# Performance work log

Hardware: AMD Instinct MI355X
Metric: run time of the kernel (lower is better)

Reference implementation:

```python
import jax, jax.numpy as jnp
import numpy as np
from jax import lax

L, H, DH, D, FF = 8, 16, 64, 1024, 4096  # layers, heads, head dim, model dim, mlp hidden
B, S = 4, 512
EPS = 1e-5


def setup_inputs() -> dict:
    key = jax.random.key(0)
    ks = jax.random.split(key, 8)
    std = 0.02
    return {
        "x": jax.random.normal(ks[0], (B, S, D), jnp.float32),
        "ln1_w": jnp.ones((L, D), jnp.float32),
        "ln1_b": jnp.zeros((L, D), jnp.float32),
        "qw": jax.random.normal(ks[1], (L, H, DH, DH), jnp.float32) * std,
        "qb": jnp.zeros((L, H, DH), jnp.float32),
        "kw": jax.random.normal(ks[2], (L, H, DH, DH), jnp.float32) * std,
        "kb": jnp.zeros((L, H, DH), jnp.float32),
        "vw": jax.random.normal(ks[3], (L, H, DH, DH), jnp.float32) * std,
        "vb": jnp.zeros((L, H, DH), jnp.float32),
        "ln2_w": jnp.ones((L, D), jnp.float32),
        "ln2_b": jnp.zeros((L, D), jnp.float32),
        "w1": jax.random.normal(ks[4], (L, D, FF), jnp.float32) * std,
        "b1": jnp.zeros((L, FF), jnp.float32),
        "w2": jax.random.normal(ks[5], (L, FF, D), jnp.float32) * std,
        "b2": jnp.zeros((L, D), jnp.float32),
    }


def _layernorm(x, w, b):
    m = jnp.mean(x, axis=-1, keepdims=True)
    v = jnp.mean(jnp.square(x - m), axis=-1, keepdims=True)
    return (x - m) * lax.rsqrt(v + EPS) * w + b


def reference(x, ln1_w, ln1_b, qw, qb, kw, kb, vw, vb, ln2_w, ln2_b, w1, b1, w2, b2):
    b, s, d = x.shape
    scale = 1.0 / jnp.sqrt(jnp.asarray(DH, x.dtype))

    def layer(h, p):
        (l1w, l1b, Qw, Qb, Kw, Kb, Vw, Vb, l2w, l2b, W1, B1, W2, B2) = p
        y = _layernorm(h, l1w, l1b)
        yh = y.reshape(b, s, H, DH)
        # nn.Linear per head: y @ W.T + b, W is [out=e, in=d]
        q = jnp.einsum('bshd,hed->bshe', yh, Qw) + Qb
        k = jnp.einsum('bshd,hed->bshe', yh, Kw) + Kb
        v = jnp.einsum('bshd,hed->bshe', yh, Vw) + Vb
        attn = jax.nn.softmax(jnp.einsum('bshe,bthe->bhst', q, k) * scale, axis=-1)
        o = jnp.einsum('bhst,bthe->bshe', attn, v).reshape(b, s, d)
        h = h + o
        z = _layernorm(h, l2w, l2b)
        z = jax.nn.gelu(z @ W1 + B1, approximate=False) @ W2 + B2
        return h + z, None

    params = (ln1_w, ln1_b, qw, qb, kw, kb, vw, vb, ln2_w, ln2_b, w1, b1, w2, b2)
    out, _ = lax.scan(layer, x, params)
    return out
```

## Files before the change

### kernel.cpp

```cpp
#include <hip/hip_runtime.h>
#include <hip/hip_bf16.h>

typedef __hip_bfloat16 bf16;
typedef __bf16 bf16x8 __attribute__((ext_vector_type(8)));
typedef float f32x4 __attribute__((ext_vector_type(4)));
typedef unsigned short u16;
typedef unsigned int u32;

#define SEQ 512
#define DMODEL 1024
#define FFDIM 4096
#define NHEAD 16
#define HDIM 64
#define NB 4
#define NLAYER 8

#define SBAR() asm volatile("s_barrier" ::: "memory")

__device__ __forceinline__ u16 f2bu(float f) {
    union { bf16 h; u16 u; } c; c.h = __float2bfloat16(f); return c.u;
}
__device__ __forceinline__ float bu2f(u16 u) {
    union { u32 i; float f; } c; c.i = ((u32)u) << 16; return c.f;
}

__device__ __forceinline__ void gload16(const bf16* g, bf16* l) {
    __builtin_amdgcn_global_load_lds(
        (const __attribute__((address_space(1))) unsigned int*)g,
        (__attribute__((address_space(3))) unsigned int*)l,
        16, 0, 0);
}

__device__ __forceinline__ void gemm_pipe(
    const bf16* __restrict__ A, int lda,
    const bf16* __restrict__ Bt,
    int nkt,
    f32x4 (&acc)[8][2],
    char* lA, char* lB)
{
    const int tid = threadIdx.x;
    const int lane = tid & 63;
    const int wave = tid >> 6;
    const int wr = wave >> 2, wc = wave & 3;
    const int l15 = lane & 15, l4 = lane >> 4;

    auto stage = [&](int c, int t) {
        const bf16* Ak = A + t * 64;
        bf16* dA = (bf16*)(lA + c * 32768);
        bf16* dB = (bf16*)(lB + c * 16384);
#pragma unroll
        for (int it = 0; it < 4; ++it) {
            const int e = (it * 512 + tid) * 8;
            const int r = e >> 6;
            const int cb = (e & 63) * 2;
            const int sc = (cb ^ (((r >> 2) & 1) << 5)) >> 1;
            gload16(Ak + (long)r * lda + sc, dA + e);
        }
        const bf16* Bk = Bt + (long)t * 8192;
#pragma unroll
        for (int it = 0; it < 2; ++it) {
            const int e = (it * 512 + tid) * 8;
            gload16(Bk + e, dB + e);
        }
    };

    stage(0, 0);
    stage(1, 1);
    asm volatile("s_waitcnt vmcnt(6)" ::: "memory");
    SBAR();

    for (int t = 0; t < nkt; ++t) {
        const int cur = t % 3;
        if (t + 2 < nkt) stage((t + 2) % 3, t + 2);

        const char* bA = lA + cur * 32768;
        const char* bB = lB + cur * 16384;

        bf16x8 bf_[2][2];
#pragma unroll
        for (int fn = 0; fn < 2; ++fn)
#pragma unroll
            for (int ks = 0; ks < 2; ++ks) {
                const int row = wc * 32 + fn * 16 + l15;
                int byte = row * 128 + (ks * 32 + l4 * 8) * 2;
                byte ^= ((row >> 2) & 1) << 5;
                bf_[fn][ks] = *(const bf16x8*)(bB + byte);
            }
#pragma unroll
        for (int q = 0; q < 4; ++q) {
            bf16x8 af[2][2];
#pragma unroll
            for (int i = 0; i < 2; ++i)
#pragma unroll
                for (int ks = 0; ks < 2; ++ks) {
                    const int row = wr * 128 + (q * 2 + i) * 16 + l15;
                    int byte = row * 128 + (ks * 32 + l4 * 8) * 2;
                    byte ^= ((row >> 2) & 1) << 5;
                    af[i][ks] = *(const bf16x8*)(bA + byte);
                }
            __builtin_amdgcn_s_setprio(1);
#pragma unroll
            for (int i = 0; i < 2; ++i)
#pragma unroll
                for (int fn = 0; fn < 2; ++fn)
#pragma unroll
                    for (int ks = 0; ks < 2; ++ks)
                        acc[q * 2 + i][fn] = __builtin_amdgcn_mfma_f32_16x16x32_bf16(
                            af[i][ks], bf_[fn][ks], acc[q * 2 + i][fn], 0, 0, 0);
            __builtin_amdgcn_s_setprio(0);
        }
        if (t + 2 < nkt) {
            asm volatile("s_waitcnt vmcnt(6)" ::: "memory");
        } else if (t + 1 < nkt) {
            asm volatile("s_waitcnt vmcnt(0)" ::: "memory");
        }
        SBAR();
    }
}

__global__ __launch_bounds__(256) void k_ln(const float* __restrict__ h,
                                            const float* __restrict__ w,
                                            const float* __restrict__ bp,
                                            bf16* __restrict__ out,
                                            float* __restrict__ hcopy)
{
    const int row = blockIdx.x;
    const int tid = threadIdx.x;
    const float4 x = ((const float4*)(h + (long)row * DMODEL))[tid];
    if (hcopy) ((float4*)(hcopy + (long)row * DMODEL))[tid] = x;
    float s  = x.x + x.y + x.z + x.w;
    float s2 = x.x * x.x + x.y * x.y + x.z * x.z + x.w * x.w;
#pragma unroll
    for (int off = 32; off; off >>= 1) { s += __shfl_xor(s, off); s2 += __shfl_xor(s2, off); }
    __shared__ float rs[4], rs2[4];
    const int wave = tid >> 6;
    if ((tid & 63) == 0) { rs[wave] = s; rs2[wave] = s2; }
    __syncthreads();
    const float S1 = rs[0] + rs[1] + rs[2] + rs[3];
    const float S2 = rs2[0] + rs2[1] + rs2[2] + rs2[3];
    const float mean = S1 * (1.0f / DMODEL);
    const float var  = S2 * (1.0f / DMODEL) - mean * mean;
    const float rstd = rsqrtf(var + 1e-5f);
    const float4 wv = ((const float4*)w)[tid];
    const float4 bv = ((const float4*)bp)[tid];
    uint2 o;
    o.x = (u32)f2bu((x.x - mean) * rstd * wv.x + bv.x) |
          ((u32)f2bu((x.y - mean) * rstd * wv.y + bv.y) << 16);
    o.y = (u32)f2bu((x.z - mean) * rstd * wv.z + bv.z) |
          ((u32)f2bu((x.w - mean) * rstd * wv.w + bv.w) << 16);
    ((uint2*)(out + (long)row * DMODEL))[tid] = o;
}

__global__ __launch_bounds__(256) void k_tilew(const float* __restrict__ w1,
                                               const float* __restrict__ w2,
                                               bf16* __restrict__ w1t,
                                               bf16* __restrict__ w2t)
{
    __shared__ u16 t[64][138];
    int bid = blockIdx.x;
    const int l = bid >> 10;
    bid &= 1023;
    const long lofs = (long)l * DMODEL * FFDIM;
    const float* src; bf16* dst; int ldsrc;
    if (bid < 512) {
        const int by = bid >> 4, kt = bid & 15;
        src = w1 + lofs + (long)(kt * 64) * FFDIM + by * 128;
        ldsrc = FFDIM;
        dst = w1t + lofs + ((long)by * 16 + kt) * 8192;
    } else {
        bid -= 512;
        const int by = bid >> 6, kt = bid & 63;
        src = w2 + lofs + (long)(kt * 64) * DMODEL + by * 128;
        ldsrc = DMODEL;
        dst = w2t + lofs + ((long)by * 64 + kt) * 8192;
    }
    const int tid = threadIdx.x;
    const int n4 = (tid & 31) * 4;
    const int kr = tid >> 5;
#pragma unroll
    for (int j = 0; j < 8; ++j) {
        const int k = j * 8 + kr;
        const float4 v = *(const float4*)(src + (long)k * ldsrc + n4);
        t[k][n4]     = f2bu(v.x);
        t[k][n4 + 1] = f2bu(v.y);
        t[k][n4 + 2] = f2bu(v.z);
        t[k][n4 + 3] = f2bu(v.w);
    }
    __syncthreads();
#pragma unroll
    for (int it = 0; it < 4; ++it) {
        const int e0 = it * 2048 + tid * 8;
        const int r = e0 >> 6;
        const int c = e0 & 63;
        const int ksw = c ^ (((r >> 2) & 1) << 4);
        u16 v[8];
#pragma unroll
        for (int m = 0; m < 8; ++m) v[m] = t[ksw + m][r];
        uint4 o;
        o.x = (u32)v[0] | ((u32)v[1] << 16);
        o.y = (u32)v[2] | ((u32)v[3] << 16);
        o.z = (u32)v[4] | ((u32)v[5] << 16);
        o.w = (u32)v[6] | ((u32)v[7] << 16);
        *(uint4*)(dst + e0) = o;
    }
}

__global__ __launch_bounds__(256) void k_attn(const bf16* __restrict__ y,
                                              const float* __restrict__ qwl,
                                              const float* __restrict__ kwl,
                                              const float* __restrict__ vwl,
                                              const float* __restrict__ qb,
                                              const float* __restrict__ kb,
                                              const float* __restrict__ vb,
                                              float* __restrict__ h)
{
    __shared__ __align__(16) char lmem[65536];
    bf16* lY  = (bf16*)lmem;
    char* lQ  = lmem + 16384;
    char* lK  = lmem + 32768;
    char* lV  = lmem + 40960;
    char* lWk = lmem + 49152;
    char* lWv = lmem + 57344;

    const int tid = threadIdx.x;
    const int lane = tid & 63, wave = tid >> 6;
    const int l15 = lane & 15, l4 = lane >> 4;
    const int z = blockIdx.y, b = z >> 4, hd = z & 15;
    const int q0 = blockIdx.x * 128;

    {
        const float* s0 = qwl + (long)hd * HDIM * HDIM;
        const float* s1 = kwl + (long)hd * HDIM * HDIM;
        const float* s2 = vwl + (long)hd * HDIM * HDIM;
#pragma unroll
        for (int it = 0; it < 4; ++it) {
            const int f = (it * 256 + tid) * 4;
            const int row = f >> 6;
            const int byte = (f << 1) ^ ((row & 7) << 4);
            float4 v = *(const float4*)(s0 + f);
            uint2 o;
            o.x = (u32)f2bu(v.x) | ((u32)f2bu(v.y) << 16);
            o.y = (u32)f2bu(v.z) | ((u32)f2bu(v.w) << 16);
            *(uint2*)(lK + byte) = o;
            v = *(const float4*)(s1 + f);
            o.x = (u32)f2bu(v.x) | ((u32)f2bu(v.y) << 16);
            o.y = (u32)f2bu(v.z) | ((u32)f2bu(v.w) << 16);
            *(uint2*)(lWk + byte) = o;
            v = *(const float4*)(s2 + f);
            o.x = (u32)f2bu(v.x) | ((u32)f2bu(v.y) << 16);
            o.y = (u32)f2bu(v.z) | ((u32)f2bu(v.w) << 16);
            *(uint2*)(lWv + byte) = o;
        }
    }
    const bf16* Yq = y + ((long)b * SEQ + q0) * DMODEL + hd * HDIM;
#pragma unroll
    for (int it = 0; it < 4; ++it) {
        const int e = (it * 256 + tid) * 8;
        const int r = e >> 6;
        const int cb = (e & 63) * 2;
        const int sc = (cb ^ (((r >> 2) & 1) << 5)) >> 1;
        gload16(Yq + (long)r * DMODEL + sc, lY + e);
    }
    __syncthreads();

    {
        f32x4 qacc[2][4] = {};
#pragma unroll
        for (int ks = 0; ks < 2; ++ks) {
            bf16x8 af[2];
#pragma unroll
            for (int fm = 0; fm < 2; ++fm) {
                const int row = wave * 32 + fm * 16 + l15;
                int byte = row * 128 + (ks * 32 + l4 * 8) * 2;
                byte ^= ((row >> 2) & 1) << 5;
                af[fm] = *(const bf16x8*)((char*)lY + byte);
            }
#pragma unroll
            for (int fn = 0; fn < 4; ++fn) {
                const int wrow = fn * 16 + l15;
                int wbyte = (wrow << 7) + ((ks * 32 + l4 * 8) << 1);
                wbyte ^= (wrow & 7) << 4;
                const bf16x8 wf = *(const bf16x8*)(lK + wbyte);
#pragma unroll
                for (int fm = 0; fm < 2; ++fm)
                    qacc[fm][fn] = __builtin_amdgcn_mfma_f32_16x16x32_bf16(
                        af[fm], wf, qacc[fm][fn], 0, 0, 0);
            }
        }
#pragma unroll
        for (int fm = 0; fm < 2; ++fm)
#pragma unroll
            for (int fn = 0; fn < 4; ++fn) {
                const int e = fn * 16 + l15;
                const float bias = qb[hd * HDIM + e];
#pragma unroll
                for (int r = 0; r < 4; ++r) {
                    const int row = wave * 32 + fm * 16 + l4 * 4 + r;
                    const int byte = ((row << 7) + (e << 1)) ^ ((row & 7) << 4);
                    *(u16*)(lQ + byte) = f2bu((qacc[fm][fn][r] + bias) * 0.125f);
                }
            }
    }
    __syncthreads();

    bf16x8 qa[2][2];
#pragma unroll
    for (int fm = 0; fm < 2; ++fm)
#pragma unroll
        for (int ks = 0; ks < 2; ++ks) {
            const int row = wave * 32 + fm * 16 + l15;
            int byte = (row << 7) + ((ks * 32 + l4 * 8) << 1);
            byte ^= (row & 7) << 4;
            qa[fm][ks] = *(const bf16x8*)(lQ + byte);
        }

    char* lP = lQ + wave * 4096;

    f32x4 O[2][4] = {};
    float mrun[2][4], lrun[2][4];
#pragma unroll
    for (int fm = 0; fm < 2; ++fm)
#pragma unroll
        for (int r = 0; r < 4; ++r) { mrun[fm][r] = -1e30f; lrun[fm][r] = 0.0f; }

    for (int kv = 0; kv < SEQ / 64; ++kv) {
        __syncthreads();
        const bf16* Ykv = y + ((long)b * SEQ + kv * 64) * DMODEL + hd * HDIM;
#pragma unroll
        for (int it = 0; it < 2; ++it) {
            const int e = (it * 256 + tid) * 8;
            const int r = e >> 6;
            const int cb = (e & 63) * 2;
            const int sc = (cb ^ (((r >> 2) & 1) << 5)) >> 1;
            gload16(Ykv + (long)r * DMODEL + sc, lY + e);
        }
        __syncthreads();

        {
            f32x4 kacc[4] = {}, vacc[4] = {};
#pragma unroll
            for (int ks = 0; ks < 2; ++ks) {
                const int yrow = wave * 16 + l15;
                int ybyte = yrow * 128 + (ks * 32 + l4 * 8) * 2;
                ybyte ^= ((yrow >> 2) & 1) << 5;
                const bf16x8 ay = *(const bf16x8*)((char*)lY + ybyte);
#pragma unroll
                for (int fn = 0; fn < 4; ++fn) {
                    const int wrow = fn * 16 + l15;
                    int wbyte = (wrow << 7) + ((ks * 32 + l4 * 8) << 1);
                    wbyte ^= (wrow & 7) << 4;
                    kacc[fn] = __builtin_amdgcn_mfma_f32_16x16x32_bf16(
                        ay, *(const bf16x8*)(lWk + wbyte), kacc[fn], 0, 0, 0);
                    vacc[fn] = __builtin_amdgcn_mfma_f32_16x16x32_bf16(
                        ay, *(const bf16x8*)(lWv + wbyte), vacc[fn], 0, 0, 0);
                }
            }
#pragma unroll
            for (int fn = 0; fn < 4; ++fn) {
                const int e = fn * 16 + l15;
                const float kbv = kb[hd * HDIM + e];
                const float vbv = vb[hd * HDIM + e];
#pragma unroll
                for (int r = 0; r < 4; ++r) {
                    const int key = wave * 16 + l4 * 4 + r;
                    const int kbyte = ((key << 7) + (e << 1)) ^ ((key & 7) << 4);
                    *(u16*)(lK + kbyte) = f2bu(kacc[fn][r] + kbv);
                    const int vbyte = ((e << 7) + (key << 1)) ^ ((e & 7) << 4);
                    *(u16*)(lV + vbyte) = f2bu(vacc[fn][r] + vbv);
                }
            }
        }
        __syncthreads();

        f32x4 sa[2][4];
#pragma unroll
        for (int fm = 0; fm < 2; ++fm)
#pragma unroll
            for (int fn = 0; fn < 4; ++fn) sa[fm][fn] = (f32x4){0.f, 0.f, 0.f, 0.f};
#pragma unroll
        for (int ks = 0; ks < 2; ++ks)
#pragma unroll
            for (int fn = 0; fn < 4; ++fn) {
                const int row = fn * 16 + l15;
                int byte = (row << 7) + ((ks * 32 + l4 * 8) << 1);
                byte ^= (row & 7) << 4;
                const bf16x8 kf = *(const bf16x8*)(lK + byte);
#pragma unroll
                for (int fm = 0; fm < 2; ++fm)
                    sa[fm][fn] = __builtin_amdgcn_mfma_f32_16x16x32_bf16(
                        qa[fm][ks], kf, sa[fm][fn], 0, 0, 0);
            }

#pragma unroll
        for (int fm = 0; fm < 2; ++fm)
#pragma unroll
            for (int r = 0; r < 4; ++r) {
                float mx = fmaxf(fmaxf(sa[fm][0][r], sa[fm][1][r]),
                                 fmaxf(sa[fm][2][r], sa[fm][3][r]));
#pragma unroll
                for (int m_ = 1; m_ < 16; m_ <<= 1) mx = fmaxf(mx, __shfl_xor(mx, m_));
                const float nm = fmaxf(mrun[fm][r], mx);
                const float al = __expf(mrun[fm][r] - nm);
                mrun[fm][r] = nm;
                float p0 = __expf(sa[fm][0][r] - nm), p1 = __expf(sa[fm][1][r] - nm);
                float p2 = __expf(sa[fm][2][r] - nm), p3 = __expf(sa[fm][3][r] - nm);
                float ps = p0 + p1 + p2 + p3;
#pragma unroll
                for (int m_ = 1; m_ < 16; m_ <<= 1) ps += __shfl_xor(ps, m_);
                lrun[fm][r] = lrun[fm][r] * al + ps;
#pragma unroll
                for (int fn = 0; fn < 4; ++fn) O[fm][fn][r] *= al;
                const int row = fm * 16 + l4 * 4 + r;
                const int rsw = (row & 7) << 4;
                const int rb_ = row << 7;
                *(u16*)(lP + ((rb_ + ((0 * 16 + l15) << 1)) ^ rsw)) = f2bu(p0);
                *(u16*)(lP + ((rb_ + ((1 * 16 + l15) << 1)) ^ rsw)) = f2bu(p1);
                *(u16*)(lP + ((rb_ + ((2 * 16 + l15) << 1)) ^ rsw)) = f2bu(p2);
                *(u16*)(lP + ((rb_ + ((3 * 16 + l15) << 1)) ^ rsw)) = f2bu(p3);
            }

#pragma unroll
        for (int ks = 0; ks < 2; ++ks) {
            bf16x8 pa[2];
#pragma unroll
            for (int fm = 0; fm < 2; ++fm) {
                const int row = fm * 16 + l15;
                int pbyte = (row << 7) + ((ks * 32 + l4 * 8) << 1);
                pbyte ^= (row & 7) << 4;
                pa[fm] = *(const bf16x8*)(lP + pbyte);
            }
#pragma unroll
            for (int fn = 0; fn < 4; ++fn) {
                const int row = fn * 16 + l15;
                int byte = (row << 7) + ((ks * 32 + l4 * 8) << 1);
                byte ^= (row & 7) << 4;
                const bf16x8 vf = *(const bf16x8*)(lV + byte);
#pragma unroll
                for (int fm = 0; fm < 2; ++fm)
                    O[fm][fn] = __builtin_amdgcn_mfma_f32_16x16x32_bf16(
                        pa[fm], vf, O[fm][fn], 0, 0, 0);
            }
        }
    }

#pragma unroll
    for (int fm = 0; fm < 2; ++fm) {
        float rinv[4];
#pragma unroll
        for (int r = 0; r < 4; ++r) rinv[r] = 1.0f / lrun[fm][r];
#pragma unroll
        for (int fn = 0; fn < 4; ++fn)
#pragma unroll
            for (int r = 0; r < 4; ++r) {
                const int qrow = q0 + wave * 32 + fm * 16 + l4 * 4 + r;
                const int e = fn * 16 + l15;
                h[((long)b * SEQ + qrow) * DMODEL + hd * HDIM + e] += O[fm][fn][r] * rinv[r];
            }
    }
}

__global__ __launch_bounds__(512, 1) void k_gemm1(const bf16* __restrict__ zb,
                                                  const bf16* __restrict__ w1t,
                                                  const float* __restrict__ b1,
                                                  bf16* __restrict__ ff1)
{
    __shared__ __align__(16) char lmem[147456];
    const int bx = (int)blockIdx.y >> 2;
    const int by = (int)blockIdx.x * 4 + ((int)blockIdx.y & 3);
    const bf16* A = zb + (long)bx * 256 * DMODEL;
    const bf16* Bt = w1t + (long)by * 16 * 8192;
    f32x4 acc[8][2] = {};
    gemm_pipe(A, DMODEL, Bt, DMODEL / 64, acc, lmem, lmem + 98304);

    const int lane = threadIdx.x & 63, wave = threadIdx.x >> 6;
    const int wr = wave >> 2, wc = wave & 3;
    const int l15 = lane & 15, l4 = lane >> 4;
#pragma unroll
    for (int fm = 0; fm < 8; ++fm)
#pragma unroll
        for (int fn = 0; fn < 2; ++fn)
#pragma unroll
            for (int r = 0; r < 4; ++r) {
                const int row = bx * 256 + wr * 128 + fm * 16 + l4 * 4 + r;
                const int col = by * 128 + wc * 32 + fn * 16 + l15;
                const float x = acc[fm][fn][r] + b1[col];
                const float g = 0.5f * x * (1.0f + erff(x * 0.70710678118f));
                ff1[(long)row * FFDIM + col] = __float2bfloat16(g);
            }
}

__global__ __launch_bounds__(512, 1) void k_gemm2(const bf16* __restrict__ ff1,
                                                  const bf16* __restrict__ w2t,
                                                  bf16* __restrict__ part)
{
    __shared__ __align__(16) char lmem[147456];
    const int sk = blockIdx.z;
    const int bx = (int)blockIdx.y;
    const int by = (int)blockIdx.x;
    const bf16* A = ff1 + (long)bx * 256 * FFDIM + (long)sk * 1024;
    const bf16* Bt = w2t + ((long)by * 64 + sk * 16) * 8192;
    f32x4 acc[8][2] = {};
    gemm_pipe(A, FFDIM, Bt, 1024 / 64, acc, lmem, lmem + 98304);

    bf16* out = part + (long)sk * (NB * SEQ) * DMODEL;
    const int lane = threadIdx.x & 63, wave = threadIdx.x >> 6;
    const int wr = wave >> 2, wc = wave & 3;
    const int l15 = lane & 15, l4 = lane >> 4;
#pragma unroll
    for (int fm = 0; fm < 8; ++fm)
#pragma unroll
        for (int fn = 0; fn < 2; ++fn)
#pragma unroll
            for (int r = 0; r < 4; ++r) {
                const int row = bx * 256 + wr * 128 + fm * 16 + l4 * 4 + r;
                const int col = by * 128 + wc * 32 + fn * 16 + l15;
                out[(long)row * DMODEL + col] = __float2bfloat16(acc[fm][fn][r]);
            }
}

__global__ __launch_bounds__(256) void k_red2ln(const bf16* __restrict__ part,
                                                const float* __restrict__ b2,
                                                float* __restrict__ h,
                                                const float* __restrict__ lnw,
                                                const float* __restrict__ lnb,
                                                bf16* __restrict__ y,
                                                int do_ln)
{
    constexpr long NELT = (long)NB * SEQ * DMODEL;
    const long row = blockIdx.x;
    const int tid = threadIdx.x;
    const long e0 = row * DMODEL + tid * 4;
    float sum[4] = {0.f, 0.f, 0.f, 0.f};
#pragma unroll
    for (int sk = 0; sk < 4; ++sk) {
        const uint2 u = *(const uint2*)(part + sk * NELT + e0);
        sum[0] += bu2f((u16)(u.x & 0xffffu));
        sum[1] += bu2f((u16)(u.x >> 16));
        sum[2] += bu2f((u16)(u.y & 0xffffu));
        sum[3] += bu2f((u16)(u.y >> 16));
    }
    const float4 bv = ((const float4*)b2)[tid];
    float4 hv = ((float4*)h)[row * (DMODEL / 4) + tid];
    hv.x += sum[0] + bv.x;
    hv.y += sum[1] + bv.y;
    hv.z += sum[2] + bv.z;
    hv.w += sum[3] + bv.w;
    ((float4*)h)[row * (DMODEL / 4) + tid] = hv;

    if (!do_ln) return;
    float ss  = hv.x + hv.y + hv.z + hv.w;
    float ss2 = hv.x * hv.x + hv.y * hv.y + hv.z * hv.z + hv.w * hv.w;
#pragma unroll
    for (int off = 32; off; off >>= 1) { ss += __shfl_xor(ss, off); ss2 += __shfl_xor(ss2, off); }
    __shared__ float rs[4], rs2[4];
    const int wave = tid >> 6;
    if ((tid & 63) == 0) { rs[wave] = ss; rs2[wave] = ss2; }
    __syncthreads();
    const float S1 = rs[0] + rs[1] + rs[2] + rs[3];
    const float S2 = rs2[0] + rs2[1] + rs2[2] + rs2[3];
    const float mean = S1 * (1.0f / DMODEL);
    const float var  = S2 * (1.0f / DMODEL) - mean * mean;
    const float rstd = rsqrtf(var + 1e-5f);
    const float4 wv = ((const float4*)lnw)[tid];
    const float4 lb = ((const float4*)lnb)[tid];
    uint2 o;
    o.x = (u32)f2bu((hv.x - mean) * rstd * wv.x + lb.x) |
          ((u32)f2bu((hv.y - mean) * rstd * wv.y + lb.y) << 16);
    o.y = (u32)f2bu((hv.z - mean) * rstd * wv.z + lb.z) |
          ((u32)f2bu((hv.w - mean) * rstd * wv.w + lb.w) << 16);
    ((uint2*)(y + row * DMODEL))[tid] = o;
}

extern "C" void kernel_launch(void* const* d_in, const int* in_sizes, int n_in,
                              void* d_out, int out_size, void* d_ws, size_t ws_size,
                              hipStream_t stream)
{
    const float* x    = (const float*)d_in[0];
    const float* ln1w = (const float*)d_in[1];
    const float* ln1b = (const float*)d_in[2];
    const float* qw   = (const float*)d_in[3];
    const float* qb   = (const float*)d_in[4];
    const float* kw   = (const float*)d_in[5];
    const float* kb   = (const float*)d_in[6];
    const float* vw   = (const float*)d_in[7];
    const float* vb   = (const float*)d_in[8];
    const float* ln2w = (const float*)d_in[9];
    const float* ln2b = (const float*)d_in[10];
    const float* w1   = (const float*)d_in[11];
    const float* b1   = (const float*)d_in[12];
    const float* w2   = (const float*)d_in[13];
    const float* b2   = (const float*)d_in[14];

    char* ws = (char*)d_ws;
    const size_t MB = 1024 * 1024;
    bf16* y    = (bf16*)(ws + 0 * MB);
    bf16* zb   = (bf16*)(ws + 4 * MB);
    bf16* ff1  = (bf16*)(ws + 20 * MB);
    bf16* part = (bf16*)(ws + 36 * MB);
    bf16* w1tA = (bf16*)(ws + 68 * MB);
    bf16* w2tA = (bf16*)(ws + 132 * MB);

    float* h = (float*)d_out;

    k_tilew<<<NLAYER * 1024, 256, 0, stream>>>(w1, w2, w1tA, w2tA);
    k_ln<<<NB * SEQ, 256, 0, stream>>>(x, ln1w, ln1b, y, h);

    for (int l = 0; l < NLAYER; ++l) {
        const long wofs = (long)l * DMODEL * FFDIM;
        k_attn<<<dim3(SEQ / 128, NB * NHEAD), 256, 0, stream>>>(
            y, qw + (long)l * 65536, kw + (long)l * 65536, vw + (long)l * 65536,
            qb + l * NHEAD * HDIM, kb + l * NHEAD * HDIM, vb + l * NHEAD * HDIM, h);
        k_ln<<<NB * SEQ, 256, 0, stream>>>(h, ln2w + l * DMODEL, ln2b + l * DMODEL, zb,
                                           nullptr);
        k_gemm1<<<dim3(8, 32), 512, 0, stream>>>(zb, w1tA + wofs, b1 + l * FFDIM, ff1);
        k_gemm2<<<dim3(8, 8, 4), 512, 0, stream>>>(ff1, w2tA + wofs, part);
        const int last = (l == NLAYER - 1);
        k_red2ln<<<NB * SEQ, 256, 0, stream>>>(part, b2 + l * DMODEL, h,
                                               ln1w + (l + 1) * DMODEL * (1 - last),
                                               ln1b + (l + 1) * DMODEL * (1 - last),
                                               y, !last);
    }
}
```

Measured before the change: 916.9 us.

## Fuse LN2, both MLP GEMMs and reduce-LN into one cooperative kernel

Replaces four per-layer launches (LayerNorm, GEMM1+GELU, split-K GEMM2, reduce+LN) with a single cooperative persistent kernel of 256 blocks that separates the phases with grid-wide syncs. The goal is to remove kernel launch gaps and tail effects between the MLP stages. In exchange it adds grid barrier overhead, drops __restrict__ on the GEMM operands, and runs the LN and reduce phases with only 256 blocks of 512 threads at 8 rows each. The 147KB static LDS allocation now also covers those LN phases, which may limit latency hiding there.

```diff
diff --git a/kernel.cpp b/kernel.cpp
--- a/kernel.cpp
+++ b/kernel.cpp
@@ -1,5 +1,8 @@
 #include <hip/hip_runtime.h>
 #include <hip/hip_bf16.h>
+#include <hip/hip_cooperative_groups.h>
+
+namespace cg = cooperative_groups;
 
 typedef __hip_bfloat16 bf16;
 typedef __bf16 bf16x8 __attribute__((ext_vector_type(8)));
@@ -32,8 +35,8 @@
 }
 
 __device__ __forceinline__ void gemm_pipe(
-    const bf16* __restrict__ A, int lda,
-    const bf16* __restrict__ Bt,
+    const bf16* A, int lda,
+    const bf16* Bt,
     int nkt,
     f32x4 (&acc)[8][2],
     char* lA, char* lB)
@@ -459,116 +462,138 @@
     }
 }
 
-__global__ __launch_bounds__(512, 1) void k_gemm1(const bf16* __restrict__ zb,
-                                                  const bf16* __restrict__ w1t,
-                                                  const float* __restrict__ b1,
-                                                  bf16* __restrict__ ff1)
+__global__ __launch_bounds__(512, 1) void k_mlp(
+    const float* ln2w, const float* ln2b,
+    float* h, bf16* zb,
+    const bf16* w1t, const float* b1, bf16* ff1,
+    const bf16* w2t, bf16* part,
+    const float* b2, const float* ln1wn, const float* ln1bn,
+    bf16* y, int do_ln)
 {
+    cg::grid_group grid = cg::this_grid();
     __shared__ __align__(16) char lmem[147456];
-    const int bx = (int)blockIdx.y >> 2;
-    const int by = (int)blockIdx.x * 4 + ((int)blockIdx.y & 3);
-    const bf16* A = zb + (long)bx * 256 * DMODEL;
-    const bf16* Bt = w1t + (long)by * 16 * 8192;
-    f32x4 acc[8][2] = {};
-    gemm_pipe(A, DMODEL, Bt, DMODEL / 64, acc, lmem, lmem + 98304);
-
-    const int lane = threadIdx.x & 63, wave = threadIdx.x >> 6;
-    const int wr = wave >> 2, wc = wave & 3;
-    const int l15 = lane & 15, l4 = lane >> 4;
-#pragma unroll
-    for (int fm = 0; fm < 8; ++fm)
-#pragma unroll
-        for (int fn = 0; fn < 2; ++fn)
-#pragma unroll
-            for (int r = 0; r < 4; ++r) {
-                const int row = bx * 256 + wr * 128 + fm * 16 + l4 * 4 + r;
-                const int col = by * 128 + wc * 32 + fn * 16 + l15;
-                const float x = acc[fm][fn][r] + b1[col];
-                const float g = 0.5f * x * (1.0f + erff(x * 0.70710678118f));
-                ff1[(long)row * FFDIM + col] = __float2bfloat16(g);
-            }
-}
-
-__global__ __launch_bounds__(512, 1) void k_gemm2(const bf16* __restrict__ ff1,
-                                                  const bf16* __restrict__ w2t,
-                                                  bf16* __restrict__ part)
-{
-    __shared__ __align__(16) char lmem[147456];
-    const int sk = blockIdx.z;
-    const int bx = (int)blockIdx.y;
-    const int by = (int)blockIdx.x;
-    const bf16* A = ff1 + (long)bx * 256 * FFDIM + (long)sk * 1024;
-    const bf16* Bt = w2t + ((long)by * 64 + sk * 16) * 8192;
-    f32x4 acc[8][2] = {};
-    gemm_pipe(A, FFDIM, Bt, 1024 / 64, acc, lmem, lmem + 98304);
-
-    bf16* out = part + (long)sk * (NB * SEQ) * DMODEL;
-    const int lane = threadIdx.x & 63, wave = threadIdx.x >> 6;
-    const int wr = wave >> 2, wc = wave & 3;
-    const int l15 = lane & 15, l4 = lane >> 4;
-#pragma unroll
-    for (int fm = 0; fm < 8; ++fm)
-#pragma unroll
-        for (int fn = 0; fn < 2; ++fn)
-#pragma unroll
-            for (int r = 0; r < 4; ++r) {
-                const int row = bx * 256 + wr * 128 + fm * 16 + l4 * 4 + r;
-                const int col = by * 128 + wc * 32 + fn * 16 + l15;
-                out[(long)row * DMODEL + col] = __float2bfloat16(acc[fm][fn][r]);
-            }
-}
-
-__global__ __launch_bounds__(256) void k_red2ln(const bf16* __restrict__ part,
-                                                const float* __restrict__ b2,
-                                                float* __restrict__ h,
-                                                const float* __restrict__ lnw,
-                                                const float* __restrict__ lnb,
-                                                bf16* __restrict__ y,
-                                                int do_ln)
-{
-    constexpr long NELT = (long)NB * SEQ * DMODEL;
-    const long row = blockIdx.x;
     const int tid = threadIdx.x;
-    const long e0 = row * DMODEL + tid * 4;
-    float sum[4] = {0.f, 0.f, 0.f, 0.f};
-#pragma unroll
-    for (int sk = 0; sk < 4; ++sk) {
-        const uint2 u = *(const uint2*)(part + sk * NELT + e0);
-        sum[0] += bu2f((u16)(u.x & 0xffffu));
-        sum[1] += bu2f((u16)(u.x >> 16));
-        sum[2] += bu2f((u16)(u.y & 0xffffu));
-        sum[3] += bu2f((u16)(u.y >> 16));
-    }
-    const float4 bv = ((const float4*)b2)[tid];
-    float4 hv = ((float4*)h)[row * (DMODEL / 4) + tid];
-    hv.x += sum[0] + bv.x;
-    hv.y += sum[1] + bv.y;
-    hv.z += sum[2] + bv.z;
-    hv.w += sum[3] + bv.w;
-    ((float4*)h)[row * (DMODEL / 4) + tid] = hv;
-
-    if (!do_ln) return;
-    float ss  = hv.x + hv.y + hv.z + hv.w;
-    float ss2 = hv.x * hv.x + hv.y * hv.y + hv.z * hv.z + hv.w * hv.w;
-#pragma unroll
-    for (int off = 32; off; off >>= 1) { ss += __shfl_xor(ss, off); ss2 += __shfl_xor(ss2, off); }
-    __shared__ float rs[4], rs2[4];
+    const int bid = blockIdx.x;
     const int wave = tid >> 6;
-    if ((tid & 63) == 0) { rs[wave] = ss; rs2[wave] = ss2; }
-    __syncthreads();
-    const float S1 = rs[0] + rs[1] + rs[2] + rs[3];
-    const float S2 = rs2[0] + rs2[1] + rs2[2] + rs2[3];
-    const float mean = S1 * (1.0f / DMODEL);
-    const float var  = S2 * (1.0f / DMODEL) - mean * mean;
-    const float rstd = rsqrtf(var + 1e-5f);
-    const float4 wv = ((const float4*)lnw)[tid];
-    const float4 lb = ((const float4*)lnb)[tid];
-    uint2 o;
-    o.x = (u32)f2bu((hv.x - mean) * rstd * wv.x + lb.x) |
-          ((u32)f2bu((hv.y - mean) * rstd * wv.y + lb.y) << 16);
-    o.y = (u32)f2bu((hv.z - mean) * rstd * wv.z + lb.z) |
-          ((u32)f2bu((hv.w - mean) * rstd * wv.w + lb.w) << 16);
-    ((uint2*)(y + row * DMODEL))[tid] = o;
+
+    {
+        float* red = (float*)lmem;
+        const float2 wv = ((const float2*)ln2w)[tid];
+        const float2 bv = ((const float2*)ln2b)[tid];
+        for (int r = 0; r < 8; ++r) {
+            const long row = (long)bid * 8 + r;
+            const float2 xv = ((const float2*)(h + row * DMODEL))[tid];
+            float s = xv.x + xv.y, s2 = xv.x * xv.x + xv.y * xv.y;
+#pragma unroll
+            for (int off = 32; off; off >>= 1) { s += __shfl_xor(s, off); s2 += __shfl_xor(s2, off); }
+            if ((tid & 63) == 0) { red[wave] = s; red[8 + wave] = s2; }
+            __syncthreads();
+            float S1 = 0.f, S2 = 0.f;
+#pragma unroll
+            for (int w = 0; w < 8; ++w) { S1 += red[w]; S2 += red[8 + w]; }
+            const float mean = S1 * (1.0f / DMODEL);
+            const float var  = S2 * (1.0f / DMODEL) - mean * mean;
+            const float rstd = rsqrtf(var + 1e-5f);
+            const u32 o = (u32)f2bu((xv.x - mean) * rstd * wv.x + bv.x) |
+                          ((u32)f2bu((xv.y - mean) * rstd * wv.y + bv.y) << 16);
+            ((u32*)(zb + row * DMODEL))[tid] = o;
+            __syncthreads();
+        }
+    }
+    grid.sync();
+
+    {
+        const int bx = bid >> 5;
+        const int by = (bid & 7) * 4 + ((bid >> 3) & 3);
+        const bf16* A = zb + (long)bx * 256 * DMODEL;
+        const bf16* Bt = w1t + (long)by * 16 * 8192;
+        f32x4 acc[8][2] = {};
+        gemm_pipe(A, DMODEL, Bt, DMODEL / 64, acc, lmem, lmem + 98304);
+
+        const int lane = tid & 63;
+        const int wr = wave >> 2, wc = wave & 3;
+        const int l15 = lane & 15, l4 = lane >> 4;
+#pragma unroll
+        for (int fm = 0; fm < 8; ++fm)
+#pragma unroll
+            for (int fn = 0; fn < 2; ++fn)
+#pragma unroll
+                for (int r = 0; r < 4; ++r) {
+                    const int row = bx * 256 + wr * 128 + fm * 16 + l4 * 4 + r;
+                    const int col = by * 128 + wc * 32 + fn * 16 + l15;
+                    const float x = acc[fm][fn][r] + b1[col];
+                    const float g = 0.5f * x * (1.0f + erff(x * 0.70710678118f));
+                    ff1[(long)row * FFDIM + col] = __float2bfloat16(g);
+                }
+    }
+    grid.sync();
+
+    {
+        const int sk = bid >> 6;
+        const int bx = (bid >> 3) & 7;
+        const int by = bid & 7;
+        const bf16* A = ff1 + (long)bx * 256 * FFDIM + (long)sk * 1024;
+        const bf16* Bt = w2t + ((long)by * 64 + sk * 16) * 8192;
+        f32x4 acc[8][2] = {};
+        gemm_pipe(A, FFDIM, Bt, 1024 / 64, acc, lmem, lmem + 98304);
+
+        bf16* out = part + (long)sk * (NB * SEQ) * DMODEL;
+        const int lane = tid & 63;
+        const int wr = wave >> 2, wc = wave & 3;
+        const int l15 = lane & 15, l4 = lane >> 4;
+#pragma unroll
+        for (int fm = 0; fm < 8; ++fm)
+#pragma unroll
+            for (int fn = 0; fn < 2; ++fn)
+#pragma unroll
+                for (int r = 0; r < 4; ++r) {
+                    const int row = bx * 256 + wr * 128 + fm * 16 + l4 * 4 + r;
+                    const int col = by * 128 + wc * 32 + fn * 16 + l15;
+                    out[(long)row * DMODEL + col] = __float2bfloat16(acc[fm][fn][r]);
+                }
+    }
+    grid.sync();
+
+    {
+        constexpr long NELT = (long)NB * SEQ * DMODEL;
+        float* red = (float*)lmem;
+        const float2 bv = ((const float2*)b2)[tid];
+        const float2 wv = ((const float2*)ln1wn)[tid];
+        const float2 lb = ((const float2*)ln1bn)[tid];
+        for (int r = 0; r < 8; ++r) {
+            const long row = (long)bid * 8 + r;
+            const long e0 = row * DMODEL + tid * 2;
+            float s0 = 0.f, s1 = 0.f;
+#pragma unroll
+            for (int sk = 0; sk < 4; ++sk) {
+                const u32 u = *(const u32*)(part + sk * NELT + e0);
+                s0 += bu2f((u16)(u & 0xffffu));
+                s1 += bu2f((u16)(u >> 16));
+            }
+            float2 hv = ((float2*)h)[row * (DMODEL / 2) + tid];
+            hv.x += s0 + bv.x;
+            hv.y += s1 + bv.y;
+            ((float2*)h)[row * (DMODEL / 2) + tid] = hv;
+
+            if (do_ln) {
+                float s = hv.x + hv.y, s2 = hv.x * hv.x + hv.y * hv.y;
+#pragma unroll
+                for (int off = 32; off; off >>= 1) { s += __shfl_xor(s, off); s2 += __shfl_xor(s2, off); }
+                if ((tid & 63) == 0) { red[wave] = s; red[8 + wave] = s2; }
+                __syncthreads();
+                float S1 = 0.f, S2 = 0.f;
+#pragma unroll
+                for (int w = 0; w < 8; ++w) { S1 += red[w]; S2 += red[8 + w]; }
+                const float mean = S1 * (1.0f / DMODEL);
+                const float var  = S2 * (1.0f / DMODEL) - mean * mean;
+                const float rstd = rsqrtf(var + 1e-5f);
+                const u32 o = (u32)f2bu((hv.x - mean) * rstd * wv.x + lb.x) |
+                              ((u32)f2bu((hv.y - mean) * rstd * wv.y + lb.y) << 16);
+                ((u32*)(y + row * DMODEL))[tid] = o;
+                __syncthreads();
+            }
+        }
+    }
 }
 
 extern "C" void kernel_launch(void* const* d_in, const int* in_sizes, int n_in,
@@ -610,14 +635,24 @@
         k_attn<<<dim3(SEQ / 128, NB * NHEAD), 256, 0, stream>>>(
             y, qw + (long)l * 65536, kw + (long)l * 65536, vw + (long)l * 65536,
             qb + l * NHEAD * HDIM, kb + l * NHEAD * HDIM, vb + l * NHEAD * HDIM, h);
-        k_ln<<<NB * SEQ, 256, 0, stream>>>(h, ln2w + l * DMODEL, ln2b + l * DMODEL, zb,
-                                           nullptr);
-        k_gemm1<<<dim3(8, 32), 512, 0, stream>>>(zb, w1tA + wofs, b1 + l * FFDIM, ff1);
-        k_gemm2<<<dim3(8, 8, 4), 512, 0, stream>>>(ff1, w2tA + wofs, part);
+
         const int last = (l == NLAYER - 1);
-        k_red2ln<<<NB * SEQ, 256, 0, stream>>>(part, b2 + l * DMODEL, h,
-                                               ln1w + (l + 1) * DMODEL * (1 - last),
-                                               ln1b + (l + 1) * DMODEL * (1 - last),
-                                               y, !last);
-    }
-}
+        const float* a_ln2w = ln2w + l * DMODEL;
+        const float* a_ln2b = ln2b + l * DMODEL;
+        float* a_h = h;
+        bf16* a_zb = zb;
+        const bf16* a_w1t = w1tA + wofs;
+        const float* a_b1 = b1 + l * FFDIM;
+        bf16* a_ff1 = ff1;
+        const bf16* a_w2t = w2tA + wofs;
+        bf16* a_part = part;
+        const float* a_b2 = b2 + l * DMODEL;
+        const float* a_ln1w = ln1w + (l + 1) * DMODEL * (1 - last);
+        const float* a_ln1b = ln1b + (l + 1) * DMODEL * (1 - last);
+        bf16* a_y = y;
+        int a_doln = !last;
+        void* args[] = {&a_ln2w, &a_ln2b, &a_h, &a_zb, &a_w1t, &a_b1, &a_ff1,
+                        &a_w2t, &a_part, &a_b2, &a_ln1w, &a_ln1b, &a_y, &a_doln};
+        hipLaunchCooperativeKernel((void*)k_mlp, dim3(256), dim3(512), args, 0, stream);
+    }
+}
```

Measured after the change: 1.796 ms. +95.9%, slower.
